# Kernel optimization log

Measured on AMD Instinct MI355X. Metric: run time of the kernel, lower is better.

The kernel has to match this reference:

```python
import jax, jax.numpy as jnp
import numpy as np

N = 50000
E = 800000
IN_DIM = 128
OUT_DIM = 128
NUM_HEADS = 4
HEAD_DIM = OUT_DIM // NUM_HEADS


def setup_inputs() -> dict:
    key = jax.random.key(0)
    ks = jax.random.split(key, 8)
    x = jax.random.normal(ks[0], (N, IN_DIM), dtype=jnp.float32)
    edge_index = jax.random.randint(ks[1], (2, E), 0, N, dtype=jnp.int64)
    # Linear(in_dim, out_dim, bias=False): store as [in, out] so h = x @ W
    s = 1.0 / np.sqrt(IN_DIM)
    W_src = jax.random.uniform(ks[2], (IN_DIM, OUT_DIM), jnp.float32, -s, s)
    W_dst = jax.random.uniform(ks[3], (IN_DIM, OUT_DIM), jnp.float32, -s, s)
    sa = 1.0 / np.sqrt(OUT_DIM)
    W_attn = jax.random.uniform(ks[4], (OUT_DIM, NUM_HEADS), jnp.float32, -sa, sa)
    ln_gamma = jnp.ones((OUT_DIM,), jnp.float32)
    ln_beta = jnp.zeros((OUT_DIM,), jnp.float32)
    return {"x": x, "edge_index": edge_index, "W_src": W_src, "W_dst": W_dst,
            "W_attn": W_attn, "ln_gamma": ln_gamma, "ln_beta": ln_beta}


def reference(x, edge_index, W_src, W_dst, W_attn, ln_gamma, ln_beta):
    n = x.shape[0]
    src_idx, dst_idx = edge_index[0], edge_index[1]
    h_src = x @ W_src                      # [N, OUT]
    h_dst = x @ W_dst                      # [N, OUT]
    hs_e = h_src[src_idx]                  # [E, OUT] gather
    a_input = hs_e + h_dst[dst_idx]        # [E, OUT]
    a = jax.nn.leaky_relu(a_input, negative_slope=0.2)
    alpha = a @ W_attn                     # [E, H]  (dropout is identity in eval)
    alpha_exp = jnp.exp(alpha - jnp.max(alpha))
    denom = jax.ops.segment_sum(alpha_exp, dst_idx, num_segments=n)  # [N, H]
    alpha_norm = alpha_exp / (denom[dst_idx] + 1e-9)                  # [E, H]
    msg = hs_e.reshape(-1, NUM_HEADS, HEAD_DIM) * alpha_norm[..., None]
    out = jax.ops.segment_sum(msg, dst_idx, num_segments=n)           # [N, H, D]
    out = out.reshape(n, OUT_DIM) + h_dst
    # LayerNorm over last dim
    mu = jnp.mean(out, axis=-1, keepdims=True)
    var = jnp.var(out, axis=-1, keepdims=True)
    return (out - mu) * jax.lax.rsqrt(var + 1e-5) * ln_gamma + ln_beta
```

## Files before the change

### kernel.cpp

```cpp
#include <hip/hip_runtime.h>
#include <math.h>

#define DIM 128
#define NHEADS 4

__global__ __launch_bounds__(256) void k_dual_gemm(
    const float* __restrict__ x,
    const float* __restrict__ Wsrc, const float* __restrict__ Wdst,
    float* __restrict__ h_src, float* __restrict__ h_dst, int n)
{
    __shared__ float xs[8][DIM];
    const int tid = threadIdx.x;
    const int r0 = blockIdx.x * 8;
    {
        int r  = tid >> 5;
        int c4 = tid & 31;
        int row = r0 + r;
        float4 v = make_float4(0.f, 0.f, 0.f, 0.f);
        if (row < n) v = ((const float4*)(x + (size_t)row * DIM))[c4];
        ((float4*)xs[r])[c4] = v;
    }
    __syncthreads();

    const int c = tid & 127;
    const float* __restrict__ W = (tid < 128) ? Wsrc : Wdst;
    float* __restrict__ H       = (tid < 128) ? h_src : h_dst;

    float acc[8] = {0.f, 0.f, 0.f, 0.f, 0.f, 0.f, 0.f, 0.f};
    #pragma unroll 2
    for (int j4 = 0; j4 < DIM / 4; ++j4) {
        const float w0 = W[(4 * j4 + 0) * DIM + c];
        const float w1 = W[(4 * j4 + 1) * DIM + c];
        const float w2 = W[(4 * j4 + 2) * DIM + c];
        const float w3 = W[(4 * j4 + 3) * DIM + c];
        #pragma unroll
        for (int r = 0; r < 8; ++r) {
            const float4 xv = ((const float4*)xs[r])[j4];
            acc[r] += xv.x * w0 + xv.y * w1 + xv.z * w2 + xv.w * w3;
        }
    }
    #pragma unroll
    for (int r = 0; r < 8; ++r) {
        if (r0 + r < n) H[(size_t)(r0 + r) * DIM + c] = acc[r];
    }
}

__global__ __launch_bounds__(256) void k_hist(
    const int* __restrict__ ei, int* __restrict__ deg, int E)
{
    int e = blockIdx.x * 256 + threadIdx.x;
    if (e < E) atomicAdd(&deg[ei[E + e]], 1);
}

__global__ __launch_bounds__(1024) void k_scanA(
    const int* __restrict__ deg, int* __restrict__ exc,
    int* __restrict__ bsum, int n)
{
    __shared__ int buf[1024];
    const int t = threadIdx.x;
    const int i = blockIdx.x * 1024 + t;
    int v = (i < n) ? deg[i] : 0;
    buf[t] = v;
    __syncthreads();
    #pragma unroll
    for (int off = 1; off < 1024; off <<= 1) {
        int u = (t >= off) ? buf[t - off] : 0;
        __syncthreads();
        buf[t] += u;
        __syncthreads();
    }
    if (i < n) exc[i] = buf[t] - v;
    if (t == 1023) bsum[blockIdx.x] = buf[1023];
}

__global__ __launch_bounds__(1024) void k_scanB(int* __restrict__ bsum, int nb)
{
    __shared__ int buf[1024];
    const int t = threadIdx.x;
    int v = (t < nb) ? bsum[t] : 0;
    buf[t] = v;
    __syncthreads();
    #pragma unroll
    for (int off = 1; off < 1024; off <<= 1) {
        int u = (t >= off) ? buf[t - off] : 0;
        __syncthreads();
        buf[t] += u;
        __syncthreads();
    }
    if (t < nb) bsum[t] = buf[t] - v;
}

__global__ __launch_bounds__(256) void k_scanC(
    const int* __restrict__ exc, const int* __restrict__ bsum,
    int* __restrict__ offs, int* __restrict__ cursor, int n, int E)
{
    int i = blockIdx.x * 256 + threadIdx.x;
    if (i < n) {
        int o = exc[i] + bsum[i >> 10];
        offs[i] = o;
        cursor[i] = o;
    }
    if (i == 0) offs[n] = E;
}

__global__ __launch_bounds__(256) void k_scatter(
    const int* __restrict__ ei, int* __restrict__ cursor,
    int* __restrict__ srcs, int E)
{
    int e = blockIdx.x * 256 + threadIdx.x;
    if (e >= E) return;
    int s = ei[e];
    int d = ei[E + e];
    int pos = atomicAdd(&cursor[d], 1);
    srcs[pos] = s;
}

__global__ __launch_bounds__(256) void k_aggregate(
    const int* __restrict__ offs, const int* __restrict__ srcs,
    const float* __restrict__ h_src, const float* __restrict__ h_dst,
    const float* __restrict__ W_attn,
    const float* __restrict__ gamma, const float* __restrict__ beta,
    float* __restrict__ out, int n)
{
    const int node = blockIdx.x * 4 + (threadIdx.x >> 6);
    if (node >= n) return;
    const int lane = threadIdx.x & 63;
    const int half = lane >> 5;
    const int l    = lane & 31;
    const int head = l >> 3;

    const float4 hd = ((const float4*)(h_dst + (size_t)node * DIM))[l];

    const float4 w0 = ((const float4*)W_attn)[4 * l + 0];
    const float4 w1 = ((const float4*)W_attn)[4 * l + 1];
    const float4 w2 = ((const float4*)W_attn)[4 * l + 2];
    const float4 w3 = ((const float4*)W_attn)[4 * l + 3];

    const int beg = offs[node];
    const int end = offs[node + 1];

    float4 acc = make_float4(0.f, 0.f, 0.f, 0.f);
    float  den = 0.f;

    for (int j = beg + half; j < end; j += 2) {
        const int s = srcs[j];
        const float4 hs = ((const float4*)(h_src + (size_t)s * DIM))[l];

        float a0 = hs.x + hd.x; a0 = a0 > 0.f ? a0 : 0.2f * a0;
        float a1 = hs.y + hd.y; a1 = a1 > 0.f ? a1 : 0.2f * a1;
        float a2 = hs.z + hd.z; a2 = a2 > 0.f ? a2 : 0.2f * a2;
        float a3 = hs.w + hd.w; a3 = a3 > 0.f ? a3 : 0.2f * a3;

        float px = a0 * w0.x + a1 * w1.x + a2 * w2.x + a3 * w3.x;
        float py = a0 * w0.y + a1 * w1.y + a2 * w2.y + a3 * w3.y;
        float pz = a0 * w0.z + a1 * w1.z + a2 * w2.z + a3 * w3.z;
        float pw = a0 * w0.w + a1 * w1.w + a2 * w2.w + a3 * w3.w;

        #pragma unroll
        for (int m = 16; m > 0; m >>= 1) {
            px += __shfl_xor(px, m, 32);
            py += __shfl_xor(py, m, 32);
            pz += __shfl_xor(pz, m, 32);
            pw += __shfl_xor(pw, m, 32);
        }

        const float ah = (head == 0) ? __expf(px) :
                         (head == 1) ? __expf(py) :
                         (head == 2) ? __expf(pz) : __expf(pw);

        acc.x += ah * hs.x;
        acc.y += ah * hs.y;
        acc.z += ah * hs.z;
        acc.w += ah * hs.w;
        den   += ah;
    }

    acc.x += __shfl_xor(acc.x, 32, 64);
    acc.y += __shfl_xor(acc.y, 32, 64);
    acc.z += __shfl_xor(acc.z, 32, 64);
    acc.w += __shfl_xor(acc.w, 32, 64);
    den   += __shfl_xor(den,   32, 64);

    const float dinv = 1.0f / (den + 1e-9f);
    float4 o;
    o.x = acc.x * dinv + hd.x;
    o.y = acc.y * dinv + hd.y;
    o.z = acc.z * dinv + hd.z;
    o.w = acc.w * dinv + hd.w;

    float s1 = o.x + o.y + o.z + o.w;
    float s2 = o.x * o.x + o.y * o.y + o.z * o.z + o.w * o.w;
    #pragma unroll
    for (int m = 16; m > 0; m >>= 1) {
        s1 += __shfl_xor(s1, m, 32);
        s2 += __shfl_xor(s2, m, 32);
    }
    const float mu   = s1 * (1.0f / 128.0f);
    const float var  = s2 * (1.0f / 128.0f) - mu * mu;
    const float rstd = rsqrtf(var + 1e-5f);

    if (half == 0) {
        const float4 g = ((const float4*)gamma)[l];
        const float4 b = ((const float4*)beta)[l];
        float4 res;
        res.x = (o.x - mu) * rstd * g.x + b.x;
        res.y = (o.y - mu) * rstd * g.y + b.y;
        res.z = (o.z - mu) * rstd * g.z + b.z;
        res.w = (o.w - mu) * rstd * g.w + b.w;
        ((float4*)(out + (size_t)node * DIM))[l] = res;
    }
}

extern "C" void kernel_launch(void* const* d_in, const int* in_sizes, int n_in,
                              void* d_out, int out_size, void* d_ws, size_t ws_size,
                              hipStream_t stream)
{
    const float* x     = (const float*)d_in[0];
    const int*   ei    = (const int*)d_in[1];
    const float* Wsrc  = (const float*)d_in[2];
    const float* Wdst  = (const float*)d_in[3];
    const float* Wattn = (const float*)d_in[4];
    const float* gamma = (const float*)d_in[5];
    const float* beta  = (const float*)d_in[6];
    float* out = (float*)d_out;

    const int n = in_sizes[0] / DIM;
    const int E = in_sizes[1] / 2;
    const int nb = (n + 1023) / 1024;

    float* h_src = (float*)d_ws;
    float* h_dst = h_src + (size_t)n * DIM;
    int*   deg    = (int*)(h_dst + (size_t)n * DIM);
    int*   offs   = deg + n;
    int*   cursor = offs + n + 1;
    int*   srcs   = cursor + n;
    int*   exc    = srcs + E;
    int*   bsum   = exc + n;

    hipMemsetAsync(deg, 0, (size_t)n * sizeof(int), stream);

    k_hist <<<(E + 255) / 256, 256, 0, stream>>>(ei, deg, E);
    k_scanA<<<nb, 1024, 0, stream>>>(deg, exc, bsum, n);
    k_scanB<<<1, 1024, 0, stream>>>(bsum, nb);
    k_scanC<<<(n + 255) / 256, 256, 0, stream>>>(exc, bsum, offs, cursor, n, E);
    k_scatter<<<(E + 255) / 256, 256, 0, stream>>>(ei, cursor, srcs, E);

    k_dual_gemm<<<(n + 7) / 8, 256, 0, stream>>>(x, Wsrc, Wdst, h_src, h_dst, n);

    k_aggregate<<<(n + 3) / 4, 256, 0, stream>>>(
        offs, srcs, h_src, h_dst, Wattn, gamma, beta, out, n);
}
```

Baseline: 359.6 us.

## Store h_src in bf16 for gather and double GEMM rows per block

The dual GEMM now writes h_src as bfloat16 while keeping h_dst in fp32, and the aggregation kernel gathers 8-byte ushort4 rows and widens them to float. This halves the bytes moved by the random per-edge gather, which is the main memory cost in aggregation. The GEMM also processes 16 rows per block instead of 8 to reuse each W load more. In exchange, attention logits and messages lose precision, and the larger accumulator array raises register pressure.

```diff
diff --git a/kernel.cpp b/kernel.cpp
--- a/kernel.cpp
+++ b/kernel.cpp
@@ -1,20 +1,29 @@
 #include <hip/hip_runtime.h>
+#include <hip/hip_bf16.h>
 #include <math.h>
 
 #define DIM 128
 #define NHEADS 4
+#define GROWS 16
+
+__device__ __forceinline__ float bf2f(unsigned short u) {
+    union { unsigned int i; float f; } v;
+    v.i = ((unsigned int)u) << 16;
+    return v.f;
+}
 
 __global__ __launch_bounds__(256) void k_dual_gemm(
     const float* __restrict__ x,
     const float* __restrict__ Wsrc, const float* __restrict__ Wdst,
-    float* __restrict__ h_src, float* __restrict__ h_dst, int n)
-{
-    __shared__ float xs[8][DIM];
+    unsigned short* __restrict__ h_srcb, float* __restrict__ h_dst, int n)
+{
+    __shared__ float xs[GROWS][DIM];
     const int tid = threadIdx.x;
-    const int r0 = blockIdx.x * 8;
-    {
-        int r  = tid >> 5;
-        int c4 = tid & 31;
+    const int r0 = blockIdx.x * GROWS;
+    #pragma unroll
+    for (int k = 0; k < GROWS * 32 / 256; ++k) {
+        int idx = k * 256 + tid;
+        int r = idx >> 5, c4 = idx & 31;
         int row = r0 + r;
         float4 v = make_float4(0.f, 0.f, 0.f, 0.f);
         if (row < n) v = ((const float4*)(x + (size_t)row * DIM))[c4];
@@ -23,10 +32,13 @@
     __syncthreads();
 
     const int c = tid & 127;
-    const float* __restrict__ W = (tid < 128) ? Wsrc : Wdst;
-    float* __restrict__ H       = (tid < 128) ? h_src : h_dst;
-
-    float acc[8] = {0.f, 0.f, 0.f, 0.f, 0.f, 0.f, 0.f, 0.f};
+    const bool is_src = (tid < 128);
+    const float* __restrict__ W = is_src ? Wsrc : Wdst;
+
+    float acc[GROWS];
+    #pragma unroll
+    for (int r = 0; r < GROWS; ++r) acc[r] = 0.f;
+
     #pragma unroll 2
     for (int j4 = 0; j4 < DIM / 4; ++j4) {
         const float w0 = W[(4 * j4 + 0) * DIM + c];
@@ -34,14 +46,24 @@
         const float w2 = W[(4 * j4 + 2) * DIM + c];
         const float w3 = W[(4 * j4 + 3) * DIM + c];
         #pragma unroll
-        for (int r = 0; r < 8; ++r) {
+        for (int r = 0; r < GROWS; ++r) {
             const float4 xv = ((const float4*)xs[r])[j4];
             acc[r] += xv.x * w0 + xv.y * w1 + xv.z * w2 + xv.w * w3;
         }
     }
-    #pragma unroll
-    for (int r = 0; r < 8; ++r) {
-        if (r0 + r < n) H[(size_t)(r0 + r) * DIM + c] = acc[r];
+    if (is_src) {
+        #pragma unroll
+        for (int r = 0; r < GROWS; ++r) {
+            if (r0 + r < n) {
+                __hip_bfloat16 b = __float2bfloat16(acc[r]);
+                h_srcb[(size_t)(r0 + r) * DIM + c] = *(unsigned short*)&b;
+            }
+        }
+    } else {
+        #pragma unroll
+        for (int r = 0; r < GROWS; ++r) {
+            if (r0 + r < n) h_dst[(size_t)(r0 + r) * DIM + c] = acc[r];
+        }
     }
 }
 
@@ -117,7 +139,7 @@
 
 __global__ __launch_bounds__(256) void k_aggregate(
     const int* __restrict__ offs, const int* __restrict__ srcs,
-    const float* __restrict__ h_src, const float* __restrict__ h_dst,
+    const unsigned short* __restrict__ h_srcb, const float* __restrict__ h_dst,
     const float* __restrict__ W_attn,
     const float* __restrict__ gamma, const float* __restrict__ beta,
     float* __restrict__ out, int n)
@@ -144,12 +166,14 @@
 
     for (int j = beg + half; j < end; j += 2) {
         const int s = srcs[j];
-        const float4 hs = ((const float4*)(h_src + (size_t)s * DIM))[l];
-
-        float a0 = hs.x + hd.x; a0 = a0 > 0.f ? a0 : 0.2f * a0;
-        float a1 = hs.y + hd.y; a1 = a1 > 0.f ? a1 : 0.2f * a1;
-        float a2 = hs.z + hd.z; a2 = a2 > 0.f ? a2 : 0.2f * a2;
-        float a3 = hs.w + hd.w; a3 = a3 > 0.f ? a3 : 0.2f * a3;
+        const ushort4 hu = ((const ushort4*)(h_srcb + (size_t)s * DIM))[l];
+        const float hx = bf2f(hu.x), hy = bf2f(hu.y),
+                    hz = bf2f(hu.z), hw = bf2f(hu.w);
+
+        float a0 = hx + hd.x; a0 = a0 > 0.f ? a0 : 0.2f * a0;
+        float a1 = hy + hd.y; a1 = a1 > 0.f ? a1 : 0.2f * a1;
+        float a2 = hz + hd.z; a2 = a2 > 0.f ? a2 : 0.2f * a2;
+        float a3 = hw + hd.w; a3 = a3 > 0.f ? a3 : 0.2f * a3;
 
         float px = a0 * w0.x + a1 * w1.x + a2 * w2.x + a3 * w3.x;
         float py = a0 * w0.y + a1 * w1.y + a2 * w2.y + a3 * w3.y;
@@ -168,10 +192,10 @@
                          (head == 1) ? __expf(py) :
                          (head == 2) ? __expf(pz) : __expf(pw);
 
-        acc.x += ah * hs.x;
-        acc.y += ah * hs.y;
-        acc.z += ah * hs.z;
-        acc.w += ah * hs.w;
+        acc.x += ah * hx;
+        acc.y += ah * hy;
+        acc.z += ah * hz;
+        acc.w += ah * hw;
         den   += ah;
     }
 
@@ -228,9 +252,9 @@
     const int E = in_sizes[1] / 2;
     const int nb = (n + 1023) / 1024;
 
-    float* h_src = (float*)d_ws;
-    float* h_dst = h_src + (size_t)n * DIM;
-    int*   deg    = (int*)(h_dst + (size_t)n * DIM);
+    float*          h_dst  = (float*)d_ws;
+    unsigned short* h_srcb = (unsigned short*)(h_dst + (size_t)n * DIM);
+    int*   deg    = (int*)(h_srcb + (size_t)n * DIM);
     int*   offs   = deg + n;
     int*   cursor = offs + n + 1;
     int*   srcs   = cursor + n;
@@ -245,8 +269,8 @@
     k_scanC<<<(n + 255) / 256, 256, 0, stream>>>(exc, bsum, offs, cursor, n, E);
     k_scatter<<<(E + 255) / 256, 256, 0, stream>>>(ei, cursor, srcs, E);
 
-    k_dual_gemm<<<(n + 7) / 8, 256, 0, stream>>>(x, Wsrc, Wdst, h_src, h_dst, n);
+    k_dual_gemm<<<(n + GROWS - 1) / GROWS, 256, 0, stream>>>(x, Wsrc, Wdst, h_srcb, h_dst, n);
 
     k_aggregate<<<(n + 3) / 4, 256, 0, stream>>>(
-        offs, srcs, h_src, h_dst, Wattn, gamma, beta, out, n);
-}
+        offs, srcs, h_srcb, h_dst, Wattn, gamma, beta, out, n);
+}
```

New measurement: 359.9 us. Within noise of the previous version (+0.1%).
